# Kernel tuning notes

Hardware: AMD Instinct MI355X
Metric: run time of the kernel (lower is better)

## Reference

```python
import jax, jax.numpy as jnp
import numpy as np


def setup_inputs() -> dict:
    key = jax.random.key(0)
    ks = jax.random.split(key, 8)
    B, H, W, C = 4, 64, 64, 256
    d = C // 8  # 32
    s = 0.02
    return {
        "x": jax.random.normal(ks[0], (B, H, W, C), dtype=jnp.float32),
        "Wq": jax.random.normal(ks[1], (C, d), dtype=jnp.float32) * s,
        "bq": jnp.zeros((d,), dtype=jnp.float32),
        "Wk": jax.random.normal(ks[2], (C, d), dtype=jnp.float32) * s,
        "bk": jnp.zeros((d,), dtype=jnp.float32),
        "Wv": jax.random.normal(ks[3], (C, C), dtype=jnp.float32) * s,
        "bv": jnp.zeros((C,), dtype=jnp.float32),
        "gamma": jnp.zeros((1,), dtype=jnp.float32),
    }


def reference(x, Wq, bq, Wk, bk, Wv, bv, gamma):
    B, H, W, C = x.shape
    N = H * W
    xf = x.reshape(B, N, C)                       # 1x1 conv == per-pixel matmul
    q = xf @ Wq + bq                              # [B, N, C//8]
    k = xf @ Wk + bk                              # [B, N, C//8]
    v = xf @ Wv + bv                              # [B, N, C]
    attn = jax.nn.softmax(jnp.einsum('bnd,bmd->bnm', q, k), axis=-1)  # [B, N, N]
    out = jnp.einsum('bnm,bmc->bnc', attn, v).reshape(B, H, W, C)
    return gamma * out + x
```

## Files before the change

kernel.cpp:

```cpp
#include <hip/hip_runtime.h>
#include <hip/hip_bf16.h>

typedef __bf16 bf16;
typedef __bf16 bf16x8 __attribute__((ext_vector_type(8)));
typedef float f32x4 __attribute__((ext_vector_type(4)));

static __device__ __forceinline__ f32x4 mfma16(bf16x8 a, bf16x8 b, f32x4 c) {
  return __builtin_amdgcn_mfma_f32_16x16x32_bf16(a, b, c, 0, 0, 0);
}

static __device__ __forceinline__ void wg_barrier() {
  asm volatile("s_waitcnt lgkmcnt(0)" ::: "memory");
  __builtin_amdgcn_s_barrier();
  asm volatile("" ::: "memory");
}

static __device__ __forceinline__ bf16x8 cvt8(const float* p) {
  f32x4 a0 = *(const f32x4*)p;
  f32x4 a1 = *(const f32x4*)(p + 4);
  bf16x8 r;
#pragma unroll
  for (int j = 0; j < 4; ++j) { r[j] = (bf16)a0[j]; r[4 + j] = (bf16)a1[j]; }
  return r;
}

__global__ void prep_wt(const float* __restrict__ Wq, const float* __restrict__ Wk,
                        const float* __restrict__ Wv, bf16* __restrict__ Wf) {
  int k = blockIdx.x;
  int c = threadIdx.x;
  float v;
  if (c < 32)       v = Wq[k * 32 + c];
  else if (c < 64)  v = Wk[k * 32 + (c - 32)];
  else              v = Wv[k * 256 + (c - 64)];
  int t5 = c >> 6, ct = (c >> 4) & 3, lwc = c & 15;
  int kc = k >> 5, qq = (k >> 3) & 3, ke = k & 7;
  Wf[((((t5 * 8 + kc) * 4 + ct) * 64) + qq * 16 + lwc) * 8 + ke] = (bf16)v;
}

__global__ __launch_bounds__(256) void qkv_gemm(
    const float* __restrict__ x, const bf16* __restrict__ Wf,
    const float* __restrict__ bq, const float* __restrict__ bk,
    const float* __restrict__ bv,
    bf16* __restrict__ Qd, bf16* __restrict__ Kd, bf16* __restrict__ Vt) {
  __shared__ __align__(16) bf16 tile[64 * 72];
  int tid = threadIdx.x;
  int lane = tid & 63, w = tid >> 6;
  int lw = lane & 15, qq = lane >> 4;
  int r0 = blockIdx.x * 64;
  int bb = r0 >> 12, n0 = r0 & 4095;

  const float* arow = x + (size_t)(r0 + 16 * w + lw) * 256;
  bf16x8 a[8];
#pragma unroll
  for (int kc = 0; kc < 8; ++kc) a[kc] = cvt8(arow + kc * 32 + qq * 8);

  for (int c0 = 0; c0 < 320; c0 += 64) {
    int t5 = c0 >> 6;
    f32x4 acc[4] = {};
#pragma unroll
    for (int kc = 0; kc < 8; ++kc)
#pragma unroll
      for (int t = 0; t < 4; ++t) {
        bf16x8 b = *(const bf16x8*)(Wf + ((size_t)(((t5 * 8 + kc) * 4 + t) * 64) + lane) * 8);
        acc[t] = mfma16(a[kc], b, acc[t]);
      }
    if (c0 == 0) {
#pragma unroll
      for (int t = 0; t < 4; ++t) {
        int c = 16 * t + lw;
        float bias = (c < 32) ? bq[c] : bk[c - 32];
#pragma unroll
        for (int i = 0; i < 4; ++i) {
          int n = n0 + 16 * w + 4 * qq + i;
          bf16 hv = (bf16)(acc[t][i] + bias);
          if (c < 32) Qd[((size_t)(bb << 12) + n) * 32 + c] = hv;
          else        Kd[((size_t)(bb << 12) + n) * 32 + (c - 32)] = hv;
        }
      }
    } else {
#pragma unroll
      for (int t = 0; t < 4; ++t) {
        int cl = 16 * t + lw;
        float bias = bv[c0 - 64 + cl];
#pragma unroll
        for (int i = 0; i < 4; ++i)
          tile[cl * 72 + 16 * w + 4 * qq + i] = (bf16)(acc[t][i] + bias);
      }
      __syncthreads();
      int nl = tid & 63;
#pragma unroll
      for (int it = 0; it < 16; ++it) {
        int cl = 4 * it + w;
        Vt[((size_t)bb * 256 + (c0 - 64) + cl) * 4096 + n0 + nl] = tile[cl * 72 + nl];
      }
      __syncthreads();
    }
  }
}

__global__ __launch_bounds__(512, 2) void flash_attn(
    const bf16* __restrict__ Qd, const bf16* __restrict__ Kd,
    const bf16* __restrict__ Vt, const float* __restrict__ x,
    const float* __restrict__ gamma, float* __restrict__ out) {
  __shared__ __align__(16) bf16 Pl[2][64 * 72];
  __shared__ __align__(16) float lsum2[2][64];

  int tid = threadIdx.x;
  int lane = tid & 63, w = tid >> 6;
  int lw = lane & 15, qq = lane >> 4;
  int wr = w & 3, wc = w >> 2, chb = 32 * w;
  int bb = blockIdx.y;
  int r0 = blockIdx.x * 64;

  const bf16* Qb = Qd + ((size_t)bb << 12) * 32;
  const bf16* Kb = Kd + ((size_t)bb << 12) * 32;
  const bf16* Vb = Vt + (size_t)bb * 256 * 4096;

  bf16x8 qf = *(const bf16x8*)(Qb + (size_t)(r0 + 16 * wr + lw) * 32 + qq * 8);

  f32x4 o[4][2] = {};
  float l_part[4] = {};
  bf16x8 kbuf0[2], kbuf1[2], vbuf0[4], vbuf1[4];

#pragma unroll
  for (int t = 0; t < 2; ++t)
    kbuf0[t] = *(const bf16x8*)(Kb + (size_t)(32 * wc + 16 * t + lw) * 32 + qq * 8);
  {
    f32x4 s[2];
#pragma unroll
    for (int t = 0; t < 2; ++t) { f32x4 z = {}; s[t] = mfma16(qf, kbuf0[t], z); }
#pragma unroll
    for (int t = 0; t < 2; ++t)
#pragma unroll
      for (int i = 0; i < 4; ++i) {
        float p = __expf(s[t][i]);
        l_part[i] += p;
        Pl[0][(16 * wr + 4 * qq + i) * 72 + 32 * wc + 16 * t + lw] = (bf16)p;
      }
  }
#pragma unroll
  for (int t = 0; t < 2; ++t)
    kbuf1[t] = *(const bf16x8*)(Kb + (size_t)(64 + 32 * wc + 16 * t + lw) * 32 + qq * 8);
#pragma unroll
  for (int t = 0; t < 2; ++t)
#pragma unroll
    for (int kc = 0; kc < 2; ++kc)
      vbuf0[t * 2 + kc] = *(const bf16x8*)(Vb + (size_t)(chb + 16 * t + lw) * 4096 + kc * 32 + qq * 8);
  wg_barrier();

#define FA_BODY(J, PCUR, PNXT, KN, KC, VC, VN)                                     \
  {                                                                                \
    const int j = (J);                                                             \
    int n1 = ((j + 1) & 63) * 64, n2 = ((j + 2) & 63) * 64;                        \
    bf16x8 af[4][2];                                                               \
    _Pragma("unroll") for (int m = 0; m < 4; ++m)                                  \
      _Pragma("unroll") for (int kc = 0; kc < 2; ++kc)                             \
        af[m][kc] = *(const bf16x8*)&Pl[PCUR][(16 * m + lw) * 72 + kc * 32 + qq * 8]; \
    if (j < 63) {                                                                  \
      f32x4 s[2];                                                                  \
      _Pragma("unroll") for (int t = 0; t < 2; ++t) {                              \
        f32x4 z = {};                                                              \
        s[t] = mfma16(qf, KN[t], z);                                               \
      }                                                                            \
      _Pragma("unroll") for (int t = 0; t < 2; ++t)                                \
        _Pragma("unroll") for (int i = 0; i < 4; ++i) {                            \
          float p = __expf(s[t][i]);                                               \
          l_part[i] += p;                                                          \
          Pl[PNXT][(16 * wr + 4 * qq + i) * 72 + 32 * wc + 16 * t + lw] = (bf16)p; \
        }                                                                          \
      _Pragma("unroll") for (int t = 0; t < 2; ++t)                                \
        KC[t] = *(const bf16x8*)(Kb + (size_t)(n2 + 32 * wc + 16 * t + lw) * 32 + qq * 8); \
    }                                                                              \
    _Pragma("unroll") for (int t = 0; t < 2; ++t)                                  \
      _Pragma("unroll") for (int kc = 0; kc < 2; ++kc)                             \
        VN[t * 2 + kc] = *(const bf16x8*)(Vb + (size_t)(chb + 16 * t + lw) * 4096 + n1 + kc * 32 + qq * 8); \
    _Pragma("unroll") for (int kc = 0; kc < 2; ++kc)                               \
      _Pragma("unroll") for (int t = 0; t < 2; ++t)                                \
        _Pragma("unroll") for (int m = 0; m < 4; ++m)                              \
          o[m][t] = mfma16(af[m][kc], VC[t * 2 + kc], o[m][t]);                    \
    wg_barrier();                                                                  \
  }

  for (int jj = 0; jj < 32; ++jj) {
    FA_BODY(2 * jj,     0, 1, kbuf1, kbuf0, vbuf0, vbuf1)
    FA_BODY(2 * jj + 1, 1, 0, kbuf0, kbuf1, vbuf1, vbuf0)
  }
#undef FA_BODY

#pragma unroll
  for (int i = 0; i < 4; ++i) {
    float v = l_part[i];
    v += __shfl_xor(v, 1);
    v += __shfl_xor(v, 2);
    v += __shfl_xor(v, 4);
    v += __shfl_xor(v, 8);
    if (lw == 0) lsum2[wc][16 * wr + 4 * qq + i] = v;
  }
  __syncthreads();

  float g = gamma[0];
#pragma unroll
  for (int m = 0; m < 4; ++m) {
    f32x4 la = *(const f32x4*)&lsum2[0][16 * m + 4 * qq];
    f32x4 lb = *(const f32x4*)&lsum2[1][16 * m + 4 * qq];
#pragma unroll
    for (int i = 0; i < 4; ++i) {
      float rinv = 1.f / (la[i] + lb[i]);
      int row = r0 + 16 * m + 4 * qq + i;
      size_t base = (((size_t)bb << 12) + row) * 256 + chb;
#pragma unroll
      for (int t = 0; t < 2; ++t)
        out[base + 16 * t + lw] = g * (o[m][t][i] * rinv) + x[base + 16 * t + lw];
    }
  }
}

extern "C" void kernel_launch(void* const* d_in, const int* in_sizes, int n_in,
                              void* d_out, int out_size, void* d_ws, size_t ws_size,
                              hipStream_t stream) {
  const float* x     = (const float*)d_in[0];
  const float* Wq    = (const float*)d_in[1];
  const float* bq    = (const float*)d_in[2];
  const float* Wk    = (const float*)d_in[3];
  const float* bk    = (const float*)d_in[4];
  const float* Wv    = (const float*)d_in[5];
  const float* bv    = (const float*)d_in[6];
  const float* gamma = (const float*)d_in[7];
  float* out = (float*)d_out;

  const size_t WT_E = 320 * 256;
  const size_t QK_E = (size_t)4096 * 32;
  const size_t VT_E = (size_t)256 * 4096;
  size_t full_bytes = (WT_E + 4 * 2 * QK_E + 4 * VT_E) * sizeof(bf16);

  bf16* Wf = (bf16*)d_ws;
  prep_wt<<<dim3(256), dim3(320), 0, stream>>>(Wq, Wk, Wv, Wf);

  if (ws_size >= full_bytes) {
    bf16* Qd = Wf + WT_E;
    bf16* Kd = Qd + 4 * QK_E;
    bf16* Vt = Kd + 4 * QK_E;
    qkv_gemm<<<dim3(256), dim3(256), 0, stream>>>(x, Wf, bq, bk, bv, Qd, Kd, Vt);
    flash_attn<<<dim3(64, 4), dim3(512), 0, stream>>>(Qd, Kd, Vt, x, gamma, out);
  } else {
    bf16* Qd = Wf + WT_E;
    bf16* Kd = Qd + QK_E;
    bf16* Vt = Kd + QK_E;
    for (int b = 0; b < 4; ++b) {
      const float* xb = x + (size_t)b * 4096 * 256;
      float* outb = out + (size_t)b * 4096 * 256;
      qkv_gemm<<<dim3(64), dim3(256), 0, stream>>>(xb, Wf, bq, bk, bv, Qd, Kd, Vt);
      flash_attn<<<dim3(64, 1), dim3(512), 0, stream>>>(Qd, Kd, Vt, xb, gamma, outb);
    }
  }
}
```

Before: 170.3 us.

## Halve flash-attention row tile to 32 to double grid and raise occupancy

Each flash_attn block now handles 32 query rows instead of 64, with the 8 waves split as 2 row groups by 4 key-column groups of 16, and the grid doubles to 128x4 blocks. Launch bounds are raised to target 4 blocks per CU, since each block needs fewer accumulator registers and half the P buffer in LDS. The intent is to fill all CUs better (512 blocks instead of 256) and hide latency with more resident waves. In exchange each block streams the full K and V once for half as many rows, so global and L2 traffic for V doubles and MFMA work per barrier drops.

```diff
diff --git a/kernel.cpp b/kernel.cpp
--- a/kernel.cpp
+++ b/kernel.cpp
@@ -98,19 +98,20 @@
   }
 }
 
-__global__ __launch_bounds__(512, 2) void flash_attn(
+__global__ __launch_bounds__(512, 4) void flash_attn(
     const bf16* __restrict__ Qd, const bf16* __restrict__ Kd,
     const bf16* __restrict__ Vt, const float* __restrict__ x,
     const float* __restrict__ gamma, float* __restrict__ out) {
-  __shared__ __align__(16) bf16 Pl[2][64 * 72];
-  __shared__ __align__(16) float lsum2[2][64];
+  __shared__ __align__(16) bf16 Pl[2][32 * 72];
+  __shared__ __align__(16) float lsum4[4][32];
 
   int tid = threadIdx.x;
   int lane = tid & 63, w = tid >> 6;
   int lw = lane & 15, qq = lane >> 4;
-  int wr = w & 3, wc = w >> 2, chb = 32 * w;
+  int wr = w & 1, wq = w >> 1;
+  int colb = 16 * wq, chb = 32 * w;
   int bb = blockIdx.y;
-  int r0 = blockIdx.x * 64;
+  int r0 = blockIdx.x * 32;
 
   const bf16* Qb = Qd + ((size_t)bb << 12) * 32;
   const bf16* Kb = Kd + ((size_t)bb << 12) * 32;
@@ -118,29 +119,22 @@
 
   bf16x8 qf = *(const bf16x8*)(Qb + (size_t)(r0 + 16 * wr + lw) * 32 + qq * 8);
 
-  f32x4 o[4][2] = {};
+  f32x4 o[2][2] = {};
   float l_part[4] = {};
-  bf16x8 kbuf0[2], kbuf1[2], vbuf0[4], vbuf1[4];
-
-#pragma unroll
-  for (int t = 0; t < 2; ++t)
-    kbuf0[t] = *(const bf16x8*)(Kb + (size_t)(32 * wc + 16 * t + lw) * 32 + qq * 8);
+  bf16x8 kbuf0, kbuf1, vbuf0[4], vbuf1[4];
+
+  kbuf0 = *(const bf16x8*)(Kb + (size_t)(colb + lw) * 32 + qq * 8);
   {
-    f32x4 s[2];
-#pragma unroll
-    for (int t = 0; t < 2; ++t) { f32x4 z = {}; s[t] = mfma16(qf, kbuf0[t], z); }
-#pragma unroll
-    for (int t = 0; t < 2; ++t)
-#pragma unroll
-      for (int i = 0; i < 4; ++i) {
-        float p = __expf(s[t][i]);
-        l_part[i] += p;
-        Pl[0][(16 * wr + 4 * qq + i) * 72 + 32 * wc + 16 * t + lw] = (bf16)p;
-      }
-  }
-#pragma unroll
-  for (int t = 0; t < 2; ++t)
-    kbuf1[t] = *(const bf16x8*)(Kb + (size_t)(64 + 32 * wc + 16 * t + lw) * 32 + qq * 8);
+    f32x4 z = {};
+    f32x4 s = mfma16(qf, kbuf0, z);
+#pragma unroll
+    for (int i = 0; i < 4; ++i) {
+      float p = __expf(s[i]);
+      l_part[i] += p;
+      Pl[0][(16 * wr + 4 * qq + i) * 72 + colb + lw] = (bf16)p;
+    }
+  }
+  kbuf1 = *(const bf16x8*)(Kb + (size_t)(64 + colb + lw) * 32 + qq * 8);
 #pragma unroll
   for (int t = 0; t < 2; ++t)
 #pragma unroll
@@ -152,31 +146,26 @@
   {                                                                                \
     const int j = (J);                                                             \
     int n1 = ((j + 1) & 63) * 64, n2 = ((j + 2) & 63) * 64;                        \
-    bf16x8 af[4][2];                                                               \
-    _Pragma("unroll") for (int m = 0; m < 4; ++m)                                  \
+    bf16x8 af[2][2];                                                               \
+    _Pragma("unroll") for (int m = 0; m < 2; ++m)                                  \
       _Pragma("unroll") for (int kc = 0; kc < 2; ++kc)                             \
         af[m][kc] = *(const bf16x8*)&Pl[PCUR][(16 * m + lw) * 72 + kc * 32 + qq * 8]; \
     if (j < 63) {                                                                  \
-      f32x4 s[2];                                                                  \
-      _Pragma("unroll") for (int t = 0; t < 2; ++t) {                              \
-        f32x4 z = {};                                                              \
-        s[t] = mfma16(qf, KN[t], z);                                               \
+      f32x4 z = {};                                                                \
+      f32x4 s = mfma16(qf, KN, z);                                                 \
+      _Pragma("unroll") for (int i = 0; i < 4; ++i) {                              \
+        float p = __expf(s[i]);                                                    \
+        l_part[i] += p;                                                            \
+        Pl[PNXT][(16 * wr + 4 * qq + i) * 72 + colb + lw] = (bf16)p;               \
       }                                                                            \
-      _Pragma("unroll") for (int t = 0; t < 2; ++t)                                \
-        _Pragma("unroll") for (int i = 0; i < 4; ++i) {                            \
-          float p = __expf(s[t][i]);                                               \
-          l_part[i] += p;                                                          \
-          Pl[PNXT][(16 * wr + 4 * qq + i) * 72 + 32 * wc + 16 * t + lw] = (bf16)p; \
-        }                                                                          \
-      _Pragma("unroll") for (int t = 0; t < 2; ++t)                                \
-        KC[t] = *(const bf16x8*)(Kb + (size_t)(n2 + 32 * wc + 16 * t + lw) * 32 + qq * 8); \
+      KC = *(const bf16x8*)(Kb + (size_t)(n2 + colb + lw) * 32 + qq * 8);          \
     }                                                                              \
     _Pragma("unroll") for (int t = 0; t < 2; ++t)                                  \
       _Pragma("unroll") for (int kc = 0; kc < 2; ++kc)                             \
         VN[t * 2 + kc] = *(const bf16x8*)(Vb + (size_t)(chb + 16 * t + lw) * 4096 + n1 + kc * 32 + qq * 8); \
     _Pragma("unroll") for (int kc = 0; kc < 2; ++kc)                               \
       _Pragma("unroll") for (int t = 0; t < 2; ++t)                                \
-        _Pragma("unroll") for (int m = 0; m < 4; ++m)                              \
+        _Pragma("unroll") for (int m = 0; m < 2; ++m)                              \
           o[m][t] = mfma16(af[m][kc], VC[t * 2 + kc], o[m][t]);                    \
     wg_barrier();                                                                  \
   }
@@ -194,18 +183,20 @@
     v += __shfl_xor(v, 2);
     v += __shfl_xor(v, 4);
     v += __shfl_xor(v, 8);
-    if (lw == 0) lsum2[wc][16 * wr + 4 * qq + i] = v;
+    if (lw == 0) lsum4[wq][16 * wr + 4 * qq + i] = v;
   }
   __syncthreads();
 
   float g = gamma[0];
 #pragma unroll
-  for (int m = 0; m < 4; ++m) {
-    f32x4 la = *(const f32x4*)&lsum2[0][16 * m + 4 * qq];
-    f32x4 lb = *(const f32x4*)&lsum2[1][16 * m + 4 * qq];
+  for (int m = 0; m < 2; ++m) {
+    f32x4 l0 = *(const f32x4*)&lsum4[0][16 * m + 4 * qq];
+    f32x4 l1 = *(const f32x4*)&lsum4[1][16 * m + 4 * qq];
+    f32x4 l2 = *(const f32x4*)&lsum4[2][16 * m + 4 * qq];
+    f32x4 l3 = *(const f32x4*)&lsum4[3][16 * m + 4 * qq];
 #pragma unroll
     for (int i = 0; i < 4; ++i) {
-      float rinv = 1.f / (la[i] + lb[i]);
+      float rinv = 1.f / (l0[i] + l1[i] + l2[i] + l3[i]);
       int row = r0 + 16 * m + 4 * qq + i;
       size_t base = (((size_t)bb << 12) + row) * 256 + chb;
 #pragma unroll
@@ -241,7 +232,7 @@
     bf16* Kd = Qd + 4 * QK_E;
     bf16* Vt = Kd + 4 * QK_E;
     qkv_gemm<<<dim3(256), dim3(256), 0, stream>>>(x, Wf, bq, bk, bv, Qd, Kd, Vt);
-    flash_attn<<<dim3(64, 4), dim3(512), 0, stream>>>(Qd, Kd, Vt, x, gamma, out);
+    flash_attn<<<dim3(128, 4), dim3(512), 0, stream>>>(Qd, Kd, Vt, x, gamma, out);
   } else {
     bf16* Qd = Wf + WT_E;
     bf16* Kd = Qd + QK_E;
@@ -250,7 +241,7 @@
       const float* xb = x + (size_t)b * 4096 * 256;
       float* outb = out + (size_t)b * 4096 * 256;
       qkv_gemm<<<dim3(64), dim3(256), 0, stream>>>(xb, Wf, bq, bk, bv, Qd, Kd, Vt);
-      flash_attn<<<dim3(64, 1), dim3(512), 0, stream>>>(Qd, Kd, Vt, xb, gamma, outb);
-    }
-  }
-}
+      flash_attn<<<dim3(128, 1), dim3(512), 0, stream>>>(Qd, Kd, Vt, xb, gamma, outb);
+    }
+  }
+}
```

Result: slower. 228.6 us (+34.2%).

## Split QKV GEMM into smaller row tiles with more waves per block

Applied to the files above, without the earlier changes.

The QKV projection kernel now handles 32 rows per block with 8 waves, split as 2 row groups by 4 column groups, each wave computing one 16x16 output tile instead of four. The grid doubles to 512 blocks, so more waves are available across the many CUs to hide the latency of global loads. The cost is that each x row is now loaded and converted by four waves instead of one, and the transposed V stores write 32-element runs instead of 64.

```diff
diff --git a/kernel.cpp b/kernel.cpp
--- a/kernel.cpp
+++ b/kernel.cpp
@@ -37,7 +37,7 @@
   Wf[((((t5 * 8 + kc) * 4 + ct) * 64) + qq * 16 + lwc) * 8 + ke] = (bf16)v;
 }
 
-__global__ __launch_bounds__(256) void qkv_gemm(
+__global__ __launch_bounds__(512, 4) void qkv_gemm(
     const float* __restrict__ x, const bf16* __restrict__ Wf,
     const float* __restrict__ bq, const float* __restrict__ bk,
     const float* __restrict__ bv,
@@ -46,52 +46,45 @@
   int tid = threadIdx.x;
   int lane = tid & 63, w = tid >> 6;
   int lw = lane & 15, qq = lane >> 4;
-  int r0 = blockIdx.x * 64;
+  int rg = w & 1, cg = w >> 1;
+  int r0 = blockIdx.x * 32;
   int bb = r0 >> 12, n0 = r0 & 4095;
 
-  const float* arow = x + (size_t)(r0 + 16 * w + lw) * 256;
+  const float* arow = x + (size_t)(r0 + 16 * rg + lw) * 256;
   bf16x8 a[8];
 #pragma unroll
   for (int kc = 0; kc < 8; ++kc) a[kc] = cvt8(arow + kc * 32 + qq * 8);
 
   for (int c0 = 0; c0 < 320; c0 += 64) {
     int t5 = c0 >> 6;
-    f32x4 acc[4] = {};
-#pragma unroll
-    for (int kc = 0; kc < 8; ++kc)
-#pragma unroll
-      for (int t = 0; t < 4; ++t) {
-        bf16x8 b = *(const bf16x8*)(Wf + ((size_t)(((t5 * 8 + kc) * 4 + t) * 64) + lane) * 8);
-        acc[t] = mfma16(a[kc], b, acc[t]);
-      }
+    f32x4 acc = {};
+#pragma unroll
+    for (int kc = 0; kc < 8; ++kc) {
+      bf16x8 b = *(const bf16x8*)(Wf + ((size_t)(((t5 * 8 + kc) * 4 + cg) * 64) + lane) * 8);
+      acc = mfma16(a[kc], b, acc);
+    }
     if (c0 == 0) {
-#pragma unroll
-      for (int t = 0; t < 4; ++t) {
-        int c = 16 * t + lw;
-        float bias = (c < 32) ? bq[c] : bk[c - 32];
-#pragma unroll
-        for (int i = 0; i < 4; ++i) {
-          int n = n0 + 16 * w + 4 * qq + i;
-          bf16 hv = (bf16)(acc[t][i] + bias);
-          if (c < 32) Qd[((size_t)(bb << 12) + n) * 32 + c] = hv;
-          else        Kd[((size_t)(bb << 12) + n) * 32 + (c - 32)] = hv;
-        }
+      int c = 16 * cg + lw;
+      float bias = (c < 32) ? bq[c] : bk[c - 32];
+#pragma unroll
+      for (int i = 0; i < 4; ++i) {
+        int n = n0 + 16 * rg + 4 * qq + i;
+        bf16 hv = (bf16)(acc[i] + bias);
+        if (c < 32) Qd[((size_t)(bb << 12) + n) * 32 + c] = hv;
+        else        Kd[((size_t)(bb << 12) + n) * 32 + (c - 32)] = hv;
       }
     } else {
-#pragma unroll
-      for (int t = 0; t < 4; ++t) {
-        int cl = 16 * t + lw;
-        float bias = bv[c0 - 64 + cl];
-#pragma unroll
-        for (int i = 0; i < 4; ++i)
-          tile[cl * 72 + 16 * w + 4 * qq + i] = (bf16)(acc[t][i] + bias);
-      }
+      int cl = 16 * cg + lw;
+      float bias = bv[c0 - 64 + cl];
+#pragma unroll
+      for (int i = 0; i < 4; ++i)
+        tile[cl * 72 + 16 * rg + 4 * qq + i] = (bf16)(acc[i] + bias);
       __syncthreads();
-      int nl = tid & 63;
-#pragma unroll
-      for (int it = 0; it < 16; ++it) {
-        int cl = 4 * it + w;
-        Vt[((size_t)bb * 256 + (c0 - 64) + cl) * 4096 + n0 + nl] = tile[cl * 72 + nl];
+#pragma unroll
+      for (int it = 0; it < 4; ++it) {
+        int ch = 16 * it + (tid >> 5);
+        int n  = tid & 31;
+        Vt[((size_t)bb * 256 + (c0 - 64) + ch) * 4096 + n0 + n] = tile[ch * 72 + n];
       }
       __syncthreads();
     }
@@ -240,7 +233,7 @@
     bf16* Qd = Wf + WT_E;
     bf16* Kd = Qd + 4 * QK_E;
     bf16* Vt = Kd + 4 * QK_E;
-    qkv_gemm<<<dim3(256), dim3(256), 0, stream>>>(x, Wf, bq, bk, bv, Qd, Kd, Vt);
+    qkv_gemm<<<dim3(512), dim3(512), 0, stream>>>(x, Wf, bq, bk, bv, Qd, Kd, Vt);
     flash_attn<<<dim3(64, 4), dim3(512), 0, stream>>>(Qd, Kd, Vt, x, gamma, out);
   } else {
     bf16* Qd = Wf + WT_E;
@@ -249,7 +242,7 @@
     for (int b = 0; b < 4; ++b) {
       const float* xb = x + (size_t)b * 4096 * 256;
       float* outb = out + (size_t)b * 4096 * 256;
-      qkv_gemm<<<dim3(64), dim3(256), 0, stream>>>(xb, Wf, bq, bk, bv, Qd, Kd, Vt);
+      qkv_gemm<<<dim3(128), dim3(512), 0, stream>>>(xb, Wf, bq, bk, bv, Qd, Kd, Vt);
       flash_attn<<<dim3(64, 1), dim3(512), 0, stream>>>(Qd, Kd, Vt, xb, gamma, outb);
     }
   }
```

Result: no change. 170.4 us (+0.1%).

## Double KV tile to 128 keys and transpose QK^T for packed P stores

Applied to the files above, without the earlier changes.

Each iteration of the flash-attention loop now covers 128 keys instead of 64, which halves the number of loop iterations and workgroup barriers. The score MFMA swaps its operands to compute K·Q^T, so each lane holds four consecutive keys and writes P to LDS as one packed bf16x4 store instead of four scalar stores. The row-sum reduction drops to two cross-lane shuffles, and P fragments are now loaded per k-chunk rather than all at once. The cost is a larger LDS buffer and roughly double the K/V prefetch registers, which could hurt occupancy under the 512x2 launch bounds.

```diff
diff --git a/kernel.cpp b/kernel.cpp
--- a/kernel.cpp
+++ b/kernel.cpp
@@ -3,6 +3,7 @@
 
 typedef __bf16 bf16;
 typedef __bf16 bf16x8 __attribute__((ext_vector_type(8)));
+typedef __bf16 bf16x4 __attribute__((ext_vector_type(4)));
 typedef float f32x4 __attribute__((ext_vector_type(4)));
 
 static __device__ __forceinline__ f32x4 mfma16(bf16x8 a, bf16x8 b, f32x4 c) {
@@ -102,7 +103,7 @@
     const bf16* __restrict__ Qd, const bf16* __restrict__ Kd,
     const bf16* __restrict__ Vt, const float* __restrict__ x,
     const float* __restrict__ gamma, float* __restrict__ out) {
-  __shared__ __align__(16) bf16 Pl[2][64 * 72];
+  __shared__ __align__(16) bf16 Pl[2][64 * 136];
   __shared__ __align__(16) float lsum2[2][64];
 
   int tid = threadIdx.x;
@@ -119,83 +120,71 @@
   bf16x8 qf = *(const bf16x8*)(Qb + (size_t)(r0 + 16 * wr + lw) * 32 + qq * 8);
 
   f32x4 o[4][2] = {};
-  float l_part[4] = {};
-  bf16x8 kbuf0[2], kbuf1[2], vbuf0[4], vbuf1[4];
-
+  float l_acc = 0.f;
+  bf16x8 kbuf0[4], kbuf1[4], vbuf0[8], vbuf1[8];
+
+#pragma unroll
+  for (int t = 0; t < 4; ++t)
+    kbuf0[t] = *(const bf16x8*)(Kb + (size_t)(64 * wc + 16 * t + lw) * 32 + qq * 8);
+#pragma unroll
+  for (int t = 0; t < 4; ++t) {
+    f32x4 z = {};
+    f32x4 s = mfma16(kbuf0[t], qf, z);
+    bf16x4 pk;
+#pragma unroll
+    for (int i = 0; i < 4; ++i) { float p = __expf(s[i]); l_acc += p; pk[i] = (bf16)p; }
+    *(bf16x4*)&Pl[0][(16 * wr + lw) * 136 + 64 * wc + 16 * t + 4 * qq] = pk;
+  }
+#pragma unroll
+  for (int t = 0; t < 4; ++t)
+    kbuf1[t] = *(const bf16x8*)(Kb + (size_t)(128 + 64 * wc + 16 * t + lw) * 32 + qq * 8);
 #pragma unroll
   for (int t = 0; t < 2; ++t)
-    kbuf0[t] = *(const bf16x8*)(Kb + (size_t)(32 * wc + 16 * t + lw) * 32 + qq * 8);
-  {
-    f32x4 s[2];
-#pragma unroll
-    for (int t = 0; t < 2; ++t) { f32x4 z = {}; s[t] = mfma16(qf, kbuf0[t], z); }
-#pragma unroll
-    for (int t = 0; t < 2; ++t)
-#pragma unroll
-      for (int i = 0; i < 4; ++i) {
-        float p = __expf(s[t][i]);
-        l_part[i] += p;
-        Pl[0][(16 * wr + 4 * qq + i) * 72 + 32 * wc + 16 * t + lw] = (bf16)p;
-      }
-  }
-#pragma unroll
-  for (int t = 0; t < 2; ++t)
-    kbuf1[t] = *(const bf16x8*)(Kb + (size_t)(64 + 32 * wc + 16 * t + lw) * 32 + qq * 8);
-#pragma unroll
-  for (int t = 0; t < 2; ++t)
-#pragma unroll
-    for (int kc = 0; kc < 2; ++kc)
-      vbuf0[t * 2 + kc] = *(const bf16x8*)(Vb + (size_t)(chb + 16 * t + lw) * 4096 + kc * 32 + qq * 8);
+#pragma unroll
+    for (int kc = 0; kc < 4; ++kc)
+      vbuf0[t * 4 + kc] = *(const bf16x8*)(Vb + (size_t)(chb + 16 * t + lw) * 4096 + kc * 32 + qq * 8);
   wg_barrier();
 
 #define FA_BODY(J, PCUR, PNXT, KN, KC, VC, VN)                                     \
   {                                                                                \
     const int j = (J);                                                             \
-    int n1 = ((j + 1) & 63) * 64, n2 = ((j + 2) & 63) * 64;                        \
-    bf16x8 af[4][2];                                                               \
-    _Pragma("unroll") for (int m = 0; m < 4; ++m)                                  \
-      _Pragma("unroll") for (int kc = 0; kc < 2; ++kc)                             \
-        af[m][kc] = *(const bf16x8*)&Pl[PCUR][(16 * m + lw) * 72 + kc * 32 + qq * 8]; \
-    if (j < 63) {                                                                  \
-      f32x4 s[2];                                                                  \
-      _Pragma("unroll") for (int t = 0; t < 2; ++t) {                              \
+    int n1 = ((j + 1) & 31) * 128, n2 = ((j + 2) & 31) * 128;                      \
+    if (j < 31) {                                                                  \
+      _Pragma("unroll") for (int t = 0; t < 4; ++t) {                              \
         f32x4 z = {};                                                              \
-        s[t] = mfma16(qf, KN[t], z);                                               \
+        f32x4 s = mfma16(KN[t], qf, z);                                            \
+        bf16x4 pk;                                                                 \
+        _Pragma("unroll") for (int i = 0; i < 4; ++i) {                            \
+          float p = __expf(s[i]); l_acc += p; pk[i] = (bf16)p;                     \
+        }                                                                          \
+        *(bf16x4*)&Pl[PNXT][(16 * wr + lw) * 136 + 64 * wc + 16 * t + 4 * qq] = pk; \
       }                                                                            \
-      _Pragma("unroll") for (int t = 0; t < 2; ++t)                                \
-        _Pragma("unroll") for (int i = 0; i < 4; ++i) {                            \
-          float p = __expf(s[t][i]);                                               \
-          l_part[i] += p;                                                          \
-          Pl[PNXT][(16 * wr + 4 * qq + i) * 72 + 32 * wc + 16 * t + lw] = (bf16)p; \
-        }                                                                          \
-      _Pragma("unroll") for (int t = 0; t < 2; ++t)                                \
-        KC[t] = *(const bf16x8*)(Kb + (size_t)(n2 + 32 * wc + 16 * t + lw) * 32 + qq * 8); \
+      _Pragma("unroll") for (int t = 0; t < 4; ++t)                                \
+        KC[t] = *(const bf16x8*)(Kb + (size_t)(n2 + 64 * wc + 16 * t + lw) * 32 + qq * 8); \
     }                                                                              \
     _Pragma("unroll") for (int t = 0; t < 2; ++t)                                  \
-      _Pragma("unroll") for (int kc = 0; kc < 2; ++kc)                             \
-        VN[t * 2 + kc] = *(const bf16x8*)(Vb + (size_t)(chb + 16 * t + lw) * 4096 + n1 + kc * 32 + qq * 8); \
-    _Pragma("unroll") for (int kc = 0; kc < 2; ++kc)                               \
+      _Pragma("unroll") for (int kc = 0; kc < 4; ++kc)                             \
+        VN[t * 4 + kc] = *(const bf16x8*)(Vb + (size_t)(chb + 16 * t + lw) * 4096 + n1 + kc * 32 + qq * 8); \
+    _Pragma("unroll") for (int kc = 0; kc < 4; ++kc) {                             \
+      bf16x8 afk[4];                                                               \
+      _Pragma("unroll") for (int m = 0; m < 4; ++m)                                \
+        afk[m] = *(const bf16x8*)&Pl[PCUR][(16 * m + lw) * 136 + kc * 32 + qq * 8]; \
       _Pragma("unroll") for (int t = 0; t < 2; ++t)                                \
         _Pragma("unroll") for (int m = 0; m < 4; ++m)                              \
-          o[m][t] = mfma16(af[m][kc], VC[t * 2 + kc], o[m][t]);                    \
+          o[m][t] = mfma16(afk[m], VC[t * 4 + kc], o[m][t]);                       \
+    }                                                                              \
     wg_barrier();                                                                  \
   }
 
-  for (int jj = 0; jj < 32; ++jj) {
+  for (int jj = 0; jj < 16; ++jj) {
     FA_BODY(2 * jj,     0, 1, kbuf1, kbuf0, vbuf0, vbuf1)
     FA_BODY(2 * jj + 1, 1, 0, kbuf0, kbuf1, vbuf1, vbuf0)
   }
 #undef FA_BODY
 
-#pragma unroll
-  for (int i = 0; i < 4; ++i) {
-    float v = l_part[i];
-    v += __shfl_xor(v, 1);
-    v += __shfl_xor(v, 2);
-    v += __shfl_xor(v, 4);
-    v += __shfl_xor(v, 8);
-    if (lw == 0) lsum2[wc][16 * wr + 4 * qq + i] = v;
-  }
+  l_acc += __shfl_xor(l_acc, 16);
+  l_acc += __shfl_xor(l_acc, 32);
+  if (qq == 0) lsum2[wc][16 * wr + lw] = l_acc;
   __syncthreads();
 
   float g = gamma[0];
```

Result: no change. 171.6 us (+0.8%).
